# Performance work log

Measured on AMD Instinct MI355X. Metric: run time of the kernel, lower is better.

## Reference

```python
import jax, jax.numpy as jnp
import numpy as np

N_NODES = 100000
IN_DIM, HID_DIM, OUT_DIM = 512, 256, 64
N_EDGES = 3200000


def setup_inputs() -> dict:
    key = jax.random.key(0)
    k1, k2, k3, k4, k5 = jax.random.split(key, 5)
    x = jax.random.normal(k1, (N_NODES, IN_DIM), dtype=jnp.float32)
    W1 = jax.random.normal(k2, (IN_DIM, HID_DIM), dtype=jnp.float32) * (1.0 / np.sqrt(IN_DIM))
    W2 = jax.random.normal(k3, (HID_DIM, OUT_DIM), dtype=jnp.float32) * (1.0 / np.sqrt(HID_DIM))
    src = jax.random.randint(k4, (N_EDGES,), 0, N_NODES, dtype=jnp.int64)
    dst = jax.random.randint(k5, (N_EDGES,), 0, N_NODES, dtype=jnp.int64)
    edge_index = jnp.stack([src, dst], axis=0)
    return {"x": x, "W1": W1, "W2": W2, "edge_index": edge_index}


def _gcn_norm(edge_index, n):
    # add self loops, symmetric normalization deg^-1/2 A_hat deg^-1/2
    loop = jnp.arange(n, dtype=edge_index.dtype)
    src = jnp.concatenate([edge_index[0], loop])
    dst = jnp.concatenate([edge_index[1], loop])
    deg = jax.ops.segment_sum(jnp.ones_like(dst, dtype=jnp.float32), dst, num_segments=n)
    dinv = jnp.where(deg > 0, jax.lax.rsqrt(deg), 0.0)
    norm = dinv[src] * dinv[dst]  # [E + N]
    return src, dst, norm


def _gcn_layer(x, W, src, dst, norm, n):
    h = x @ W                       # dense projection [N, D_out]
    msg = h[src] * norm[:, None]    # gather + scale  [E+N, D_out]
    return jax.ops.segment_sum(msg, dst, num_segments=n)  # scatter-add [N, D_out]


def reference(x, W1, W2, edge_index):
    n = x.shape[0]
    src, dst, norm = _gcn_norm(edge_index, n)
    # dropout p=0.0 -> identity (inference reference)
    h = _gcn_layer(x, W1, src, dst, norm, n)
    h = jax.nn.relu(h)
    out = _gcn_layer(h, W2, src, dst, norm, n)
    return out
```

## Files before the change

### kernel.cpp

```cpp
#include <hip/hip_runtime.h>


typedef short s16x8 __attribute__((ext_vector_type(8)));
typedef float f32x4 __attribute__((ext_vector_type(4)));

static constexpr int IN_DIM = 512;
static constexpr int HID = 256;
static constexpr int OUTD = 64;

static constexpr int BKT_SHIFT = 8;
static constexpr int MAX_NB = 400;
static constexpr int CAP_BIN = 32;
static constexpr int EDGES_PER_BLOCK = 8192;
static constexpr int SEG_CAP = 16384;

static __device__ __forceinline__ float bf2f(unsigned short u) {
  unsigned int x = ((unsigned int)u) << 16;
  float f;
  __builtin_memcpy(&f, &x, 4);
  return f;
}
static __device__ __forceinline__ unsigned short f2bf(float f) {
  unsigned int x;
  __builtin_memcpy(&x, &f, 4);
  unsigned int r = x + 0x7fffu + ((x >> 16) & 1u);
  return (unsigned short)(r >> 16);
}
static __device__ __forceinline__ float ub(unsigned int x, int k) {
  return (float)((x >> (8 * k)) & 0xffu);
}

__global__ __launch_bounds__(256) void pack_init_kernel(
    const float* __restrict__ W1, const float* __restrict__ W2,
    short* __restrict__ Wt1, short* __restrict__ Wt2,
    unsigned* __restrict__ bucket_cursor) {
  int idx = blockIdx.x * blockDim.x + threadIdx.x;
  if (idx < IN_DIM * HID) {
    int n = idx / IN_DIM, k = idx - n * IN_DIM;
    Wt1[idx] = (short)f2bf(W1[(size_t)k * HID + n]);
  }
  if (idx < HID * OUTD) {
    int n = idx / HID, k = idx - n * HID;
    Wt2[idx] = (short)f2bf(W2[(size_t)k * OUTD + n]);
  }
  if (idx < 512) bucket_cursor[idx] = (unsigned)idx * SEG_CAP;
}

__global__ __launch_bounds__(256) void scatter_kernel(
    const int* __restrict__ src, const int* __restrict__ dst, int E,
    unsigned* __restrict__ bucket_cursor, unsigned* __restrict__ entry_buf) {
  __shared__ unsigned cnt[MAX_NB];
  __shared__ unsigned poss[MAX_NB];
  __shared__ unsigned buf[MAX_NB * CAP_BIN];
  const int tid = threadIdx.x;
  const int e0 = blockIdx.x * EDGES_PER_BLOCK;
  const int e1 = min(E, e0 + EDGES_PER_BLOCK);
  for (int i = tid; i < MAX_NB; i += 256) cnt[i] = 0;
  __syncthreads();
  for (int e = e0 + tid; e < e1; e += 256) {
    int d = dst[e];
    unsigned entry = (((unsigned)src[e]) << 8) | ((unsigned)d & 255u);
    int bkt = d >> BKT_SHIFT;
    unsigned slot = atomicAdd(&cnt[bkt], 1u);
    if (slot < CAP_BIN) {
      buf[bkt * CAP_BIN + slot] = entry;
    } else {
      unsigned pos = atomicAdd(&bucket_cursor[bkt], 1u);
      entry_buf[pos] = entry;
    }
  }
  __syncthreads();
  for (int b = tid; b < MAX_NB; b += 256) {
    unsigned c = min(cnt[b], (unsigned)CAP_BIN);
    poss[b] = c ? atomicAdd(&bucket_cursor[b], c) : 0u;
  }
  __syncthreads();
  for (int b0 = 0; b0 < MAX_NB; b0 += 8) {
    int b = b0 + (tid >> 5);
    int i = tid & 31;
    unsigned c = min(cnt[b], (unsigned)CAP_BIN);
    if ((unsigned)i < c) entry_buf[poss[b] + i] = buf[b * CAP_BIN + i];
  }
}

__global__ __launch_bounds__(256) void build_kernel(
    const unsigned* __restrict__ entry_buf,
    const unsigned* __restrict__ bucket_cursor, int Nn,
    int* __restrict__ csr_src, unsigned* __restrict__ row_start,
    unsigned* __restrict__ row_cnt, float* __restrict__ dinv) {
  __shared__ unsigned hist[256];
  __shared__ unsigned scn[256];
  const int tid = threadIdx.x;
  const int b = blockIdx.x;
  const unsigned nb0 = (unsigned)b * SEG_CAP;
  const int n_e = (int)(bucket_cursor[b] - nb0);

  hist[tid] = 0;
  __syncthreads();
  for (int i = tid; i < n_e; i += 256)
    atomicAdd(&hist[entry_buf[nb0 + i] & 255u], 1u);
  __syncthreads();

  unsigned v = hist[tid];
  scn[tid] = v;
  __syncthreads();
  for (int off = 1; off < 256; off <<= 1) {
    unsigned t = (tid >= off) ? scn[tid - off] : 0u;
    __syncthreads();
    scn[tid] += t;
    __syncthreads();
  }
  unsigned excl = scn[tid] - v;
  __syncthreads();
  scn[tid] = excl;

  int node = (b << BKT_SHIFT) + tid;
  if (node < Nn) {
    dinv[node] = rsqrtf((float)v + 1.0f);
    row_start[node] = nb0 + excl;
    row_cnt[node] = v;
  }
  hist[tid] = 0;
  __syncthreads();

  for (int i = tid; i < n_e; i += 256) {
    unsigned en = entry_buf[nb0 + i];
    unsigned d = en & 255u;
    unsigned r = atomicAdd(&hist[d], 1u);
    csr_src[nb0 + scn[d] + r] = (int)(en >> 8);
  }
}

template <int BM, int BN, int WGM, int WGN, bool A_F32>
__launch_bounds__(256)
__global__ void gemm_kernel(const void* __restrict__ Av,
                            const short* __restrict__ Bt,
                            short* __restrict__ C, int M, int K,
                            const float* __restrict__ dinv) {
  constexpr int BK = 32;
  constexpr int N = BN;
  __shared__ short sA[BM * BK];
  __shared__ short sB[BN * BK];
  const int tid = threadIdx.x;
  const int wave = tid >> 6, lane = tid & 63;
  const int lm = lane & 15, lq = lane >> 4;
  const int row0 = blockIdx.x * BM;
  const int wm0 = (WGM > 1) ? wave * 64 : 0;
  const int wn0 = (WGN > 1) ? wave * 64 : 0;

  f32x4 acc[4][4];
#pragma unroll
  for (int i = 0; i < 4; i++)
#pragma unroll
    for (int j = 0; j < 4; j++) acc[i][j] = f32x4{0.f, 0.f, 0.f, 0.f};

  for (int k0 = 0; k0 < K; k0 += BK) {
    if constexpr (A_F32) {
      static_assert(BM == 64, "fp32 A staging assumes BM=64");
      const float* A = (const float*)Av;
      int m = tid >> 2, kc = tid & 3;
      int row = row0 + m;
      float4 f0 = make_float4(0, 0, 0, 0), f1 = f0;
      if (row < M) {
        const float4* pa = (const float4*)(A + (size_t)row * K + k0 + kc * 8);
        f0 = pa[0];
        f1 = pa[1];
      }
      s16x8 v;
      v[0] = (short)f2bf(f0.x); v[1] = (short)f2bf(f0.y);
      v[2] = (short)f2bf(f0.z); v[3] = (short)f2bf(f0.w);
      v[4] = (short)f2bf(f1.x); v[5] = (short)f2bf(f1.y);
      v[6] = (short)f2bf(f1.z); v[7] = (short)f2bf(f1.w);
      *(s16x8*)&sA[m * BK + kc * 8] = v;
    } else {
      const short* A = (const short*)Av;
#pragma unroll
      for (int i = 0; i < BM / 64; i++) {
        int idx = tid + i * 256;
        int m = idx >> 2, kc = idx & 3;
        int row = row0 + m;
        s16x8 v = {0, 0, 0, 0, 0, 0, 0, 0};
        if (row < M) v = *(const s16x8*)(A + (size_t)row * K + k0 + kc * 8);
        *(s16x8*)&sA[m * BK + kc * 8] = v;
      }
    }
#pragma unroll
    for (int i = 0; i < BN / 64; i++) {
      int idx = tid + i * 256;
      int n = idx >> 2, kc = idx & 3;
      *(s16x8*)&sB[n * BK + kc * 8] =
          *(const s16x8*)(Bt + (size_t)n * K + k0 + kc * 8);
    }
    __syncthreads();

    s16x8 af[4], bfr[4];
#pragma unroll
    for (int mi = 0; mi < 4; mi++)
      af[mi] = *(const s16x8*)&sA[(wm0 + mi * 16 + lm) * BK + lq * 8];
#pragma unroll
    for (int ni = 0; ni < 4; ni++)
      bfr[ni] = *(const s16x8*)&sB[(wn0 + ni * 16 + lm) * BK + lq * 8];
#pragma unroll
    for (int mi = 0; mi < 4; mi++)
#pragma unroll
      for (int ni = 0; ni < 4; ni++)
        acc[mi][ni] = __builtin_amdgcn_mfma_f32_16x16x32_bf16(
            af[mi], bfr[ni], acc[mi][ni], 0, 0, 0);
    __syncthreads();
  }

#pragma unroll
  for (int mi = 0; mi < 4; mi++)
#pragma unroll
    for (int r = 0; r < 4; r++) {
      int row = row0 + wm0 + mi * 16 + lq * 4 + r;
      if (row < M) {
        float di = dinv[row];
#pragma unroll
        for (int ni = 0; ni < 4; ni++) {
          int col = wn0 + ni * 16 + lm;
          C[(size_t)row * N + col] = (short)f2bf(acc[mi][ni][r] * di);
        }
      }
    }
}

template <int D>
__global__ __launch_bounds__(256) void quant_kernel(
    const short* __restrict__ h, unsigned char* __restrict__ q,
    float* __restrict__ scale, int n) {
  constexpr int T = D / 4;
  constexpr int RPB = 256 / T;
  int row = blockIdx.x * RPB + threadIdx.x / T;
  if (row >= n) return;
  int t = threadIdx.x % T;
  short4 v = *(const short4*)(h + (size_t)row * D + t * 4);
  float f0 = bf2f((unsigned short)v.x), f1 = bf2f((unsigned short)v.y);
  float f2 = bf2f((unsigned short)v.z), f3 = bf2f((unsigned short)v.w);
  float m = fmaxf(fmaxf(fabsf(f0), fabsf(f1)), fmaxf(fabsf(f2), fabsf(f3)));
#pragma unroll
  for (int mk = 1; mk < T; mk <<= 1) m = fmaxf(m, __shfl_xor(m, mk));
  float inv = 127.0f / fmaxf(m, 1e-30f);
  uchar4 o;
  o.x = (unsigned char)((int)rintf(f0 * inv) + 128);
  o.y = (unsigned char)((int)rintf(f1 * inv) + 128);
  o.z = (unsigned char)((int)rintf(f2 * inv) + 128);
  o.w = (unsigned char)((int)rintf(f3 * inv) + 128);
  *(uchar4*)(q + (size_t)row * D + t * 4) = o;
  if (t == 0) scale[row] = m * (1.0f / 127.0f);
}

__global__ __launch_bounds__(256) void agg1_kernel(
    const unsigned char* __restrict__ q1, const float* __restrict__ qs,
    const float* __restrict__ dinv,
    const unsigned* __restrict__ row_start, const unsigned* __restrict__ row_cnt,
    const int* __restrict__ csr_src, short* __restrict__ out, int n) {
  int node = blockIdx.x * 4 + (threadIdx.x >> 6);
  if (node >= n) return;
  const int lane = threadIdx.x & 63;
  const int half = lane >> 5;
  const int d0 = (lane & 31) * 8;
  float a[8];
#pragma unroll
  for (int j = 0; j < 8; j++) a[j] = 0.f;
  float K = 0.f;
  if (half == 0) {
    uint2 v = *(const uint2*)(q1 + (size_t)node * HID + d0);
    float w = qs[node];
    K += w;
#pragma unroll
    for (int j = 0; j < 4; j++) {
      a[j] += ub(v.x, j) * w;
      a[j + 4] += ub(v.y, j) * w;
    }
  }
  unsigned e = row_start[node] + half;
  const unsigned e1 = row_start[node] + row_cnt[node];
  for (; e + 6 < e1; e += 8) {
    int s0 = csr_src[e], s1 = csr_src[e + 2];
    int s2 = csr_src[e + 4], s3 = csr_src[e + 6];
    float w0 = qs[s0], w1 = qs[s1], w2 = qs[s2], w3 = qs[s3];
    uint2 v0 = *(const uint2*)(q1 + (size_t)s0 * HID + d0);
    uint2 v1 = *(const uint2*)(q1 + (size_t)s1 * HID + d0);
    uint2 v2 = *(const uint2*)(q1 + (size_t)s2 * HID + d0);
    uint2 v3 = *(const uint2*)(q1 + (size_t)s3 * HID + d0);
    K += (w0 + w1) + (w2 + w3);
#pragma unroll
    for (int j = 0; j < 4; j++) {
      a[j] += ub(v0.x, j) * w0 + ub(v1.x, j) * w1 + ub(v2.x, j) * w2 +
              ub(v3.x, j) * w3;
      a[j + 4] += ub(v0.y, j) * w0 + ub(v1.y, j) * w1 + ub(v2.y, j) * w2 +
                  ub(v3.y, j) * w3;
    }
  }
  for (; e < e1; e += 2) {
    int s0 = csr_src[e];
    float w0 = qs[s0];
    uint2 v0 = *(const uint2*)(q1 + (size_t)s0 * HID + d0);
    K += w0;
#pragma unroll
    for (int j = 0; j < 4; j++) {
      a[j] += ub(v0.x, j) * w0;
      a[j + 4] += ub(v0.y, j) * w0;
    }
  }
#pragma unroll
  for (int j = 0; j < 8; j++) a[j] += __shfl_xor(a[j], 32);
  K += __shfl_xor(K, 32);
  if (half == 0) {
    const float di = dinv[node];
    const float bias = 128.0f * K;
    s16x8 o;
#pragma unroll
    for (int j = 0; j < 8; j++)
      o[j] = (short)f2bf(fmaxf((a[j] - bias) * di, 0.f));
    *(s16x8*)(out + (size_t)node * HID + d0) = o;
  }
}

__global__ __launch_bounds__(256) void agg2_kernel(
    const unsigned char* __restrict__ q2, const float* __restrict__ qs,
    const float* __restrict__ dinv,
    const unsigned* __restrict__ row_start, const unsigned* __restrict__ row_cnt,
    const int* __restrict__ csr_src, float* __restrict__ out, int n) {
  int node = blockIdx.x * 4 + (threadIdx.x >> 6);
  if (node >= n) return;
  const int lane = threadIdx.x & 63;
  const int q = lane >> 4;
  const int d0 = (lane & 15) * 4;
  float a[4] = {0.f, 0.f, 0.f, 0.f};
  float K = 0.f;
  if (q == 0) {
    unsigned v = *(const unsigned*)(q2 + (size_t)node * OUTD + d0);
    float w = qs[node];
    K += w;
#pragma unroll
    for (int j = 0; j < 4; j++) a[j] += ub(v, j) * w;
  }
  unsigned e = row_start[node] + q;
  const unsigned e1 = row_start[node] + row_cnt[node];
  for (; e + 12 < e1; e += 16) {
    int s0 = csr_src[e], s1 = csr_src[e + 4];
    int s2 = csr_src[e + 8], s3 = csr_src[e + 12];
    float w0 = qs[s0], w1 = qs[s1], w2 = qs[s2], w3 = qs[s3];
    unsigned v0 = *(const unsigned*)(q2 + (size_t)s0 * OUTD + d0);
    unsigned v1 = *(const unsigned*)(q2 + (size_t)s1 * OUTD + d0);
    unsigned v2 = *(const unsigned*)(q2 + (size_t)s2 * OUTD + d0);
    unsigned v3 = *(const unsigned*)(q2 + (size_t)s3 * OUTD + d0);
    K += (w0 + w1) + (w2 + w3);
#pragma unroll
    for (int j = 0; j < 4; j++)
      a[j] += (ub(v0, j) * w0 + ub(v1, j) * w1) +
              (ub(v2, j) * w2 + ub(v3, j) * w3);
  }
  for (; e < e1; e += 4) {
    int s0 = csr_src[e];
    float w0 = qs[s0];
    unsigned v0 = *(const unsigned*)(q2 + (size_t)s0 * OUTD + d0);
    K += w0;
#pragma unroll
    for (int j = 0; j < 4; j++) a[j] += ub(v0, j) * w0;
  }
#pragma unroll
  for (int j = 0; j < 4; j++) {
    a[j] += __shfl_xor(a[j], 16);
    a[j] += __shfl_xor(a[j], 32);
  }
  K += __shfl_xor(K, 16);
  K += __shfl_xor(K, 32);
  if (q == 0) {
    const float di = dinv[node];
    const float bias = 128.0f * K;
    float4 o = make_float4((a[0] - bias) * di, (a[1] - bias) * di,
                           (a[2] - bias) * di, (a[3] - bias) * di);
    *(float4*)(out + (size_t)node * OUTD + d0) = o;
  }
}


extern "C" void kernel_launch(void* const* d_in, const int* in_sizes, int n_in,
                              void* d_out, int out_size, void* d_ws,
                              size_t ws_size, hipStream_t stream) {
  const float* x = (const float*)d_in[0];
  const float* W1 = (const float*)d_in[1];
  const float* W2 = (const float*)d_in[2];
  const int* ei = (const int*)d_in[3];
  const int E = in_sizes[3] / 2;
  const int Nn = in_sizes[0] / IN_DIM;
  const int* src = ei;
  const int* dst = ei + E;
  const int NB = (Nn + 255) >> BKT_SHIFT;

  char* p = (char*)d_ws;
  auto alloc = [&](size_t bytes) {
    char* r = p;
    p += (bytes + 255) & ~(size_t)255;
    return r;
  };
  unsigned* bucket_cursor = (unsigned*)alloc(512 * 4);
  unsigned* row_start = (unsigned*)alloc((size_t)Nn * 4);
  unsigned* row_cnt = (unsigned*)alloc((size_t)Nn * 4);
  float* dinv = (float*)alloc((size_t)Nn * 4);
  float* qs1 = (float*)alloc((size_t)Nn * 4);
  float* qs2 = (float*)alloc((size_t)Nn * 4);
  int* csr_src = (int*)alloc((size_t)MAX_NB * SEG_CAP * 4);
  unsigned* entry_buf = (unsigned*)alloc((size_t)MAX_NB * SEG_CAP * 4);
  short* Wt1 = (short*)alloc((size_t)IN_DIM * HID * 2);
  short* Wt2 = (short*)alloc((size_t)HID * OUTD * 2);
  short* h1 = (short*)alloc((size_t)Nn * HID * 2);
  short* agg1 = (short*)alloc((size_t)Nn * HID * 2);
  unsigned char* q1 = (unsigned char*)entry_buf;
  short* h2 = (short*)entry_buf;
  unsigned char* q2 = (unsigned char*)entry_buf + (16u << 20);

  pack_init_kernel<<<(IN_DIM * HID + 255) / 256, 256, 0, stream>>>(
      W1, W2, Wt1, Wt2, bucket_cursor);
  scatter_kernel<<<(E + EDGES_PER_BLOCK - 1) / EDGES_PER_BLOCK, 256, 0,
                   stream>>>(src, dst, E, bucket_cursor, entry_buf);
  build_kernel<<<NB, 256, 0, stream>>>(entry_buf, bucket_cursor, Nn, csr_src,
                                       row_start, row_cnt, dinv);
  gemm_kernel<64, 256, 1, 4, true>
      <<<(Nn + 63) / 64, 256, 0, stream>>>(x, Wt1, h1, Nn, IN_DIM, dinv);
  quant_kernel<HID><<<(Nn + 3) / 4, 256, 0, stream>>>(h1, q1, qs1, Nn);
  agg1_kernel<<<(Nn + 3) / 4, 256, 0, stream>>>(q1, qs1, dinv, row_start,
                                                row_cnt, csr_src, agg1, Nn);
  gemm_kernel<256, 64, 4, 1, false>
      <<<(Nn + 255) / 256, 256, 0, stream>>>(agg1, Wt2, h2, Nn, HID, dinv);
  quant_kernel<OUTD><<<(Nn + 15) / 16, 256, 0, stream>>>(h2, q2, qs2, Nn);
  agg2_kernel<<<(Nn + 3) / 4, 256, 0, stream>>>(q2, qs2, dinv, row_start,
                                                row_cnt, csr_src,
                                                (float*)d_out, Nn);
}
```

Before: 622.0 us.

## Fuse per-row int8 quantization into both GEMM epilogues and drop quant kernels

Both dense projection kernels now compute the per-row absolute max in their epilogue and write int8 codes plus a row scale directly, so the bf16 intermediates h1/h2 and the two separate quant kernels go away. The first GEMM is retiled to 128x256 with 512 threads and uses an LDS atomicMax to combine the row max across its four column waves. This removes a full write and reread of the N x 256 and N x 64 intermediates plus two launches. In exchange the epilogues get heavier, and the quantized values are now taken from fp32 accumulators rather than bf16-rounded values, so they can differ slightly.

New measurement: 595.3 us. 1.04x faster.

```diff
diff --git a/kernel.cpp b/kernel.cpp
--- a/kernel.cpp
+++ b/kernel.cpp
@@ -131,22 +131,22 @@
   }
 }
 
-template <int BM, int BN, int WGM, int WGN, bool A_F32>
-__launch_bounds__(256)
-__global__ void gemm_kernel(const void* __restrict__ Av,
-                            const short* __restrict__ Bt,
-                            short* __restrict__ C, int M, int K,
-                            const float* __restrict__ dinv) {
-  constexpr int BK = 32;
-  constexpr int N = BN;
+__global__ __launch_bounds__(512) void gemm1_kernel(
+    const float* __restrict__ A, const short* __restrict__ Bt,
+    unsigned char* __restrict__ q, float* __restrict__ qscale,
+    const float* __restrict__ dinv, int M) {
+  constexpr int K = IN_DIM;
+  constexpr int BN = HID;
+  constexpr int BM = 128, BK = 32;
   __shared__ short sA[BM * BK];
   __shared__ short sB[BN * BK];
+  __shared__ int rmax[BM];
   const int tid = threadIdx.x;
   const int wave = tid >> 6, lane = tid & 63;
   const int lm = lane & 15, lq = lane >> 4;
   const int row0 = blockIdx.x * BM;
-  const int wm0 = (WGM > 1) ? wave * 64 : 0;
-  const int wn0 = (WGN > 1) ? wave * 64 : 0;
+  const int wm0 = (wave >> 2) * 64;
+  const int wn0 = (wave & 3) * 64;
 
   f32x4 acc[4][4];
 #pragma unroll
@@ -155,9 +155,7 @@
     for (int j = 0; j < 4; j++) acc[i][j] = f32x4{0.f, 0.f, 0.f, 0.f};
 
   for (int k0 = 0; k0 < K; k0 += BK) {
-    if constexpr (A_F32) {
-      static_assert(BM == 64, "fp32 A staging assumes BM=64");
-      const float* A = (const float*)Av;
+    {
       int m = tid >> 2, kc = tid & 3;
       int row = row0 + m;
       float4 f0 = make_float4(0, 0, 0, 0), f1 = f0;
@@ -172,21 +170,10 @@
       v[4] = (short)f2bf(f1.x); v[5] = (short)f2bf(f1.y);
       v[6] = (short)f2bf(f1.z); v[7] = (short)f2bf(f1.w);
       *(s16x8*)&sA[m * BK + kc * 8] = v;
-    } else {
-      const short* A = (const short*)Av;
-#pragma unroll
-      for (int i = 0; i < BM / 64; i++) {
-        int idx = tid + i * 256;
-        int m = idx >> 2, kc = idx & 3;
-        int row = row0 + m;
-        s16x8 v = {0, 0, 0, 0, 0, 0, 0, 0};
-        if (row < M) v = *(const s16x8*)(A + (size_t)row * K + k0 + kc * 8);
-        *(s16x8*)&sA[m * BK + kc * 8] = v;
-      }
-    }
-#pragma unroll
-    for (int i = 0; i < BN / 64; i++) {
-      int idx = tid + i * 256;
+    }
+#pragma unroll
+    for (int i = 0; i < 2; i++) {
+      int idx = tid + i * 512;
       int n = idx >> 2, kc = idx & 3;
       *(s16x8*)&sB[n * BK + kc * 8] =
           *(const s16x8*)(Bt + (size_t)n * K + k0 + kc * 8);
@@ -209,45 +196,120 @@
     __syncthreads();
   }
 
+  for (int i = tid; i < BM; i += 512) rmax[i] = 0;
+  __syncthreads();
+#pragma unroll
+  for (int mi = 0; mi < 4; mi++)
+#pragma unroll
+    for (int r = 0; r < 4; r++) {
+      int lrow = wm0 + mi * 16 + lq * 4 + r;
+      int row = row0 + lrow;
+      float di = (row < M) ? dinv[row] : 0.f;
+      float mx = 0.f;
+#pragma unroll
+      for (int ni = 0; ni < 4; ni++) mx = fmaxf(mx, fabsf(acc[mi][ni][r]));
+      mx *= di;
+#pragma unroll
+      for (int w = 1; w < 16; w <<= 1) mx = fmaxf(mx, __shfl_xor(mx, w));
+      if (lm == 0) atomicMax(&rmax[lrow], __float_as_int(mx));
+    }
+  __syncthreads();
+#pragma unroll
+  for (int mi = 0; mi < 4; mi++)
+#pragma unroll
+    for (int r = 0; r < 4; r++) {
+      int lrow = wm0 + mi * 16 + lq * 4 + r;
+      int row = row0 + lrow;
+      if (row >= M) continue;
+      float di = dinv[row];
+      float rm = __int_as_float(rmax[lrow]);
+      float inv = 127.0f / fmaxf(rm, 1e-30f);
+#pragma unroll
+      for (int ni = 0; ni < 4; ni++) {
+        int col = wn0 + ni * 16 + lm;
+        int qv = (int)rintf(acc[mi][ni][r] * di * inv) + 128;
+        q[(size_t)row * BN + col] = (unsigned char)qv;
+      }
+      if (wn0 == 0 && lm == 0) qscale[row] = rm * (1.0f / 127.0f);
+    }
+}
+
+__global__ __launch_bounds__(256) void gemm2_kernel(
+    const short* __restrict__ A, const short* __restrict__ Bt,
+    unsigned char* __restrict__ q, float* __restrict__ qscale,
+    const float* __restrict__ dinv, int M) {
+  constexpr int K = HID;
+  constexpr int BN = OUTD;
+  constexpr int BM = 256, BK = 32;
+  __shared__ short sA[BM * BK];
+  __shared__ short sB[BN * BK];
+  const int tid = threadIdx.x;
+  const int wave = tid >> 6, lane = tid & 63;
+  const int lm = lane & 15, lq = lane >> 4;
+  const int row0 = blockIdx.x * BM;
+  const int wm0 = wave * 64;
+
+  f32x4 acc[4][4];
+#pragma unroll
+  for (int i = 0; i < 4; i++)
+#pragma unroll
+    for (int j = 0; j < 4; j++) acc[i][j] = f32x4{0.f, 0.f, 0.f, 0.f};
+
+  for (int k0 = 0; k0 < K; k0 += BK) {
+#pragma unroll
+    for (int i = 0; i < 4; i++) {
+      int idx = tid + i * 256;
+      int m = idx >> 2, kc = idx & 3;
+      int row = row0 + m;
+      s16x8 v = {0, 0, 0, 0, 0, 0, 0, 0};
+      if (row < M) v = *(const s16x8*)(A + (size_t)row * K + k0 + kc * 8);
+      *(s16x8*)&sA[m * BK + kc * 8] = v;
+    }
+    {
+      int n = tid >> 2, kc = tid & 3;
+      *(s16x8*)&sB[n * BK + kc * 8] =
+          *(const s16x8*)(Bt + (size_t)n * K + k0 + kc * 8);
+    }
+    __syncthreads();
+
+    s16x8 af[4], bfr[4];
+#pragma unroll
+    for (int mi = 0; mi < 4; mi++)
+      af[mi] = *(const s16x8*)&sA[(wm0 + mi * 16 + lm) * BK + lq * 8];
+#pragma unroll
+    for (int ni = 0; ni < 4; ni++)
+      bfr[ni] = *(const s16x8*)&sB[(ni * 16 + lm) * BK + lq * 8];
+#pragma unroll
+    for (int mi = 0; mi < 4; mi++)
+#pragma unroll
+      for (int ni = 0; ni < 4; ni++)
+        acc[mi][ni] = __builtin_amdgcn_mfma_f32_16x16x32_bf16(
+            af[mi], bfr[ni], acc[mi][ni], 0, 0, 0);
+    __syncthreads();
+  }
+
 #pragma unroll
   for (int mi = 0; mi < 4; mi++)
 #pragma unroll
     for (int r = 0; r < 4; r++) {
       int row = row0 + wm0 + mi * 16 + lq * 4 + r;
-      if (row < M) {
-        float di = dinv[row];
-#pragma unroll
-        for (int ni = 0; ni < 4; ni++) {
-          int col = wn0 + ni * 16 + lm;
-          C[(size_t)row * N + col] = (short)f2bf(acc[mi][ni][r] * di);
-        }
+      if (row >= M) continue;
+      float di = dinv[row];
+      float mx = 0.f;
+#pragma unroll
+      for (int ni = 0; ni < 4; ni++) mx = fmaxf(mx, fabsf(acc[mi][ni][r]));
+      mx *= di;
+#pragma unroll
+      for (int w = 1; w < 16; w <<= 1) mx = fmaxf(mx, __shfl_xor(mx, w));
+      float inv = 127.0f / fmaxf(mx, 1e-30f);
+#pragma unroll
+      for (int ni = 0; ni < 4; ni++) {
+        int col = ni * 16 + lm;
+        int qv = (int)rintf(acc[mi][ni][r] * di * inv) + 128;
+        q[(size_t)row * BN + col] = (unsigned char)qv;
       }
-    }
-}
-
-template <int D>
-__global__ __launch_bounds__(256) void quant_kernel(
-    const short* __restrict__ h, unsigned char* __restrict__ q,
-    float* __restrict__ scale, int n) {
-  constexpr int T = D / 4;
-  constexpr int RPB = 256 / T;
-  int row = blockIdx.x * RPB + threadIdx.x / T;
-  if (row >= n) return;
-  int t = threadIdx.x % T;
-  short4 v = *(const short4*)(h + (size_t)row * D + t * 4);
-  float f0 = bf2f((unsigned short)v.x), f1 = bf2f((unsigned short)v.y);
-  float f2 = bf2f((unsigned short)v.z), f3 = bf2f((unsigned short)v.w);
-  float m = fmaxf(fmaxf(fabsf(f0), fabsf(f1)), fmaxf(fabsf(f2), fabsf(f3)));
-#pragma unroll
-  for (int mk = 1; mk < T; mk <<= 1) m = fmaxf(m, __shfl_xor(m, mk));
-  float inv = 127.0f / fmaxf(m, 1e-30f);
-  uchar4 o;
-  o.x = (unsigned char)((int)rintf(f0 * inv) + 128);
-  o.y = (unsigned char)((int)rintf(f1 * inv) + 128);
-  o.z = (unsigned char)((int)rintf(f2 * inv) + 128);
-  o.w = (unsigned char)((int)rintf(f3 * inv) + 128);
-  *(uchar4*)(q + (size_t)row * D + t * 4) = o;
-  if (t == 0) scale[row] = m * (1.0f / 127.0f);
+      if (lm == 0) qscale[row] = mx * (1.0f / 127.0f);
+    }
 }
 
 __global__ __launch_bounds__(256) void agg1_kernel(
@@ -407,10 +469,8 @@
   unsigned* entry_buf = (unsigned*)alloc((size_t)MAX_NB * SEG_CAP * 4);
   short* Wt1 = (short*)alloc((size_t)IN_DIM * HID * 2);
   short* Wt2 = (short*)alloc((size_t)HID * OUTD * 2);
-  short* h1 = (short*)alloc((size_t)Nn * HID * 2);
   short* agg1 = (short*)alloc((size_t)Nn * HID * 2);
   unsigned char* q1 = (unsigned char*)entry_buf;
-  short* h2 = (short*)entry_buf;
   unsigned char* q2 = (unsigned char*)entry_buf + (16u << 20);
 
   pack_init_kernel<<<(IN_DIM * HID + 255) / 256, 256, 0, stream>>>(
@@ -419,14 +479,12 @@
                    stream>>>(src, dst, E, bucket_cursor, entry_buf);
   build_kernel<<<NB, 256, 0, stream>>>(entry_buf, bucket_cursor, Nn, csr_src,
                                        row_start, row_cnt, dinv);
-  gemm_kernel<64, 256, 1, 4, true>
-      <<<(Nn + 63) / 64, 256, 0, stream>>>(x, Wt1, h1, Nn, IN_DIM, dinv);
-  quant_kernel<HID><<<(Nn + 3) / 4, 256, 0, stream>>>(h1, q1, qs1, Nn);
+  gemm1_kernel<<<(Nn + 127) / 128, 512, 0, stream>>>(x, Wt1, q1, qs1, dinv,
+                                                     Nn);
   agg1_kernel<<<(Nn + 3) / 4, 256, 0, stream>>>(q1, qs1, dinv, row_start,
                                                 row_cnt, csr_src, agg1, Nn);
-  gemm_kernel<256, 64, 4, 1, false>
-      <<<(Nn + 255) / 256, 256, 0, stream>>>(agg1, Wt2, h2, Nn, HID, dinv);
-  quant_kernel<OUTD><<<(Nn + 15) / 16, 256, 0, stream>>>(h2, q2, qs2, Nn);
+  gemm2_kernel<<<(Nn + 255) / 256, 256, 0, stream>>>(agg1, Wt2, q2, qs2, dinv,
+                                                     Nn);
   agg2_kernel<<<(Nn + 3) / 4, 256, 0, stream>>>(q2, qs2, dinv, row_start,
                                                 row_cnt, csr_src,
                                                 (float*)d_out, Nn);
```
